# Kernel tuning notes

Hardware: AMD Instinct MI355X
Metric: run time of the kernel (lower is better)

Reference implementation:

```python
import jax, jax.numpy as jnp
import numpy as np

N_SPECIAL = 4
LABEL_ID = 3
C_ACT = 64
C_TIME = 32
ACT_START = N_SPECIAL
TIME_START = N_SPECIAL + C_ACT
VOCAB = TIME_START + C_TIME  # 100
B, T, D = 8, 2048, 256


def l2norm(x, eps=1e-12):
    n = jnp.sqrt(jnp.sum(x * x, axis=-1, keepdims=True))
    return x / jnp.maximum(n, eps)


def causal_proto(h_norm, is_label, nxt, lo, hi, E_cls, alpha):
    """At every <LABEL> position L, build per-class prototypes from earlier
    support label positions (class = next token at that position), add a
    Bayesian prior alpha*E_cls, and return cosine sims of h_norm[L] vs protos.
    Non-label positions (or labels with no earlier support) -> zeros.
    Implemented as a single causal scan over time (online running sums)."""
    Bv, Tv, Dv = h_norm.shape
    C = E_cls.shape[0]
    is_sup = is_label & (nxt >= lo) & (nxt < hi)          # [B,T]
    cls = jnp.clip(nxt - lo, 0, C - 1)                    # [B,T]

    def step(carry, xs):
        Hsum, cnt = carry                                  # [B,C,D], [B,C]
        h_t, cls_t, sup_t, lab_t = xs                      # [B,D],[B],[B],[B]
        proto = l2norm((Hsum + alpha * E_cls) / (cnt[:, :, None] + alpha + 1e-8))
        sims = jnp.einsum('bd,bcd->bc', h_t, proto)        # cosine (h_t is unit)
        valid = lab_t & (jnp.sum(cnt, axis=-1) > 0)        # any earlier support
        out = jnp.where(valid[:, None], sims, 0.0)
        oh = jax.nn.one_hot(cls_t, C, dtype=h_t.dtype) * sup_t[:, None].astype(h_t.dtype)
        Hsum = Hsum + oh[:, :, None] * h_t[:, None, :]
        cnt = cnt + oh
        return (Hsum, cnt), out

    init = (jnp.zeros((Bv, C, Dv), h_norm.dtype), jnp.zeros((Bv, C), h_norm.dtype))
    xs = (jnp.swapaxes(h_norm, 0, 1), jnp.swapaxes(cls, 0, 1),
          jnp.swapaxes(is_sup, 0, 1), jnp.swapaxes(is_label, 0, 1))
    _, outs = jax.lax.scan(jax.checkpoint(step), init, xs)
    return jnp.swapaxes(outs, 0, 1)                        # [B,T,C]


def setup_inputs() -> dict:
    key = jax.random.key(0)
    ks = jax.random.split(key, 6)
    f32 = jnp.float32
    return {
        'tokens': jax.random.randint(ks[0], (B, T), 0, VOCAB, dtype=jnp.int32),
        'h': jax.random.normal(ks[1], (B, T, D), dtype=f32),
        'E': jax.random.normal(ks[2], (VOCAB, D), dtype=f32) * 0.02,
        'W_next': jax.random.normal(ks[3], (C_ACT, D), dtype=f32) * 0.02,
        'b_next': jnp.zeros((C_ACT,), f32),
        'W_time': jax.random.normal(ks[4], (C_TIME, D), dtype=f32) * 0.02,
        'b_time': jnp.zeros((C_TIME,), f32),
        'tied_scale_act': jnp.array(0.0, f32),
        'tied_scale_time': jnp.array(0.0, f32),
        'proto_scale_act': jnp.array(1.0, f32),
        'proto_scale_time': jnp.array(1.0, f32),
        'proto_prior_act': jnp.array(0.5, f32),
        'proto_prior_time': jnp.array(0.5, f32),
        'proto_temp_act': jnp.array(1.0, f32),
        'proto_temp_time': jnp.array(1.0, f32),
    }


def reference(tokens, h, E, W_next, b_next, W_time, b_time,
              tied_scale_act, tied_scale_time, proto_scale_act, proto_scale_time,
              proto_prior_act, proto_prior_time, proto_temp_act, proto_temp_time):
    sp = jax.nn.softplus
    # parametric heads
    param_next = jnp.einsum('btd,cd->btc', h, W_next) + b_next
    param_time = jnp.einsum('btd,cd->btc', h, W_time) + b_time
    # weight-tied heads (gradient flows into E here)
    tied_act = jnp.einsum('btd,cd->btc', h, E[ACT_START:TIME_START])
    tied_time = jnp.einsum('btd,cd->btc', h, E[TIME_START:VOCAB])
    # prototype head (E detached, as in the torch code)
    h_norm = l2norm(h)
    E_det = jax.lax.stop_gradient(E)
    E_act = l2norm(E_det[ACT_START:TIME_START])
    E_time = l2norm(E_det[TIME_START:VOCAB])
    nxt = jnp.roll(tokens, -1, axis=1)
    is_label = tokens == LABEL_ID
    proto_act = causal_proto(h_norm, is_label, nxt, ACT_START, TIME_START,
                             E_act, sp(proto_prior_act)) * sp(proto_temp_act)
    proto_time = causal_proto(h_norm, is_label, nxt, TIME_START, VOCAB,
                              E_time, sp(proto_prior_time)) * sp(proto_temp_time)
    activity_logits = param_next + sp(tied_scale_act) * tied_act + sp(proto_scale_act) * proto_act
    time_logits = param_time + sp(tied_scale_time) * tied_time + sp(proto_scale_time) * proto_time
    return (activity_logits, time_logits)
```

## Files before the change

### kernel.cpp

```cpp
#include <hip/hip_runtime.h>
#include <hip/hip_bf16.h>

#define Bv 8
#define Tv 2048
#define Dv 256
#define C_ACT 64
#define C_TIME 32
#define NCLS 96
#define LABEL_ID 3
#define ACT_START 4
#define TIME_START 68
#define VOCAB 100
#define MAXEV 36

typedef short bf16x8 __attribute__((ext_vector_type(8)));
typedef float f32x4  __attribute__((ext_vector_type(4)));
typedef unsigned short u16x8 __attribute__((ext_vector_type(8)));

__device__ __forceinline__ float bf2f(__hip_bfloat16 x) { return __bfloat162float(x); }
__device__ __forceinline__ float bfb(unsigned short u) {
    union { unsigned int i; float f; } x; x.i = ((unsigned int)u) << 16; return x.f;
}
__device__ __forceinline__ short f2bs(float x) {
    __hip_bfloat16 b = __float2bfloat16(x);
    return *reinterpret_cast<short*>(&b);
}
__device__ __forceinline__ float spf(float x) { return log1pf(expf(x)); }

__device__ __forceinline__ float ldx(const void* p, size_t i, bool f32) {
    return f32 ? ((const float*)p)[i] : bf2f(((const __hip_bfloat16*)p)[i]);
}
__device__ __forceinline__ void stx(void* p, size_t i, float v, bool f32) {
    if (f32) ((float*)p)[i] = v;
    else     ((__hip_bfloat16*)p)[i] = __float2bfloat16(v);
}
__device__ __forceinline__ float4 ld4(const void* p, size_t i, bool f32) {
    if (f32) return *reinterpret_cast<const float4*>((const float*)p + i);
    ushort4 s = *reinterpret_cast<const ushort4*>((const unsigned short*)p + i);
    float4 u; u.x = bfb(s.x); u.y = bfb(s.y); u.z = bfb(s.z); u.w = bfb(s.w);
    return u;
}

__device__ __forceinline__ bool detect_f32_256(const void* h, int tid, int* s_cnt)
{
    if (tid == 0) *s_cnt = 0;
    __syncthreads();
    ushort4 u = *(reinterpret_cast<const ushort4*>(h) + tid);
    int c = 0; float v;
    v = bfb(u.x); if (!(fabsf(v) < 1e20f)) c++;
    v = bfb(u.y); if (!(fabsf(v) < 1e20f)) c++;
    v = bfb(u.z); if (!(fabsf(v) < 1e20f)) c++;
    v = bfb(u.w); if (!(fabsf(v) < 1e20f)) c++;
    #pragma unroll
    for (int o = 32; o > 0; o >>= 1) c += __shfl_down(c, o);
    if ((tid & 63) == 0 && c) atomicAdd(s_cnt, c);
    __syncthreads();
    return *s_cnt >= 4;
}

__device__ __forceinline__ size_t out_idx(int b, int L, int c)
{
    return (c < C_ACT)
        ? ((size_t)(b * Tv + L) * C_ACT + c)
        : ((size_t)Bv * Tv * C_ACT + (size_t)(b * Tv + L) * C_TIME + (c - C_ACT));
}

#define K1_ROWS 32
#define EVLD 264
#define GLD 44

__global__ __launch_bounds__(256) void k_all(
    const int* __restrict__ tokens,
    const void* __restrict__ h,
    const void* __restrict__ E,
    const void* __restrict__ Wn, const void* __restrict__ bn,
    const void* __restrict__ Wt, const void* __restrict__ bt,
    const void* ts_a, const void* ts_t,
    const void* ps_a, const void* ps_t,
    const void* pp_a, const void* pp_t,
    const void* pt_a, const void* pt_t,
    void* __restrict__ out)
{
    __shared__ union {
        unsigned short mB[NCLS][EVLD];
        struct {
            unsigned short hb[48][EVLD];
            union {
                unsigned short AsMs[48][EVLD];
                struct {
                    float Gl[MAXEV][GLD];
                    float P[MAXEV][24];
                    float Pm[MAXEV][24];
                    float SG[MAXEV][24];
                    float ZP[MAXEV][24];
                } r;
            } u2;
            float nrm[MAXEV];
        } s;
    } u;
    __shared__ int s_pos[MAXEV], s_cls[MAXEV];
    __shared__ unsigned long long s_mask[32];
    __shared__ unsigned long long s_bm[24];
    __shared__ unsigned long long s_mact, s_mtim;
    __shared__ int s_cnt, s_evn;

    int tid = threadIdx.x;
    bool f32 = detect_f32_256(h, tid, &s_cnt);
    float spt_a = spf(ldx(ts_a, 0, f32));
    float spt_t = spf(ldx(ts_t, 0, f32));

    if (blockIdx.x >= 32) {
        int R0   = (blockIdx.x - 32) * K1_ROWS;
        int w    = tid >> 6;
        int lane = tid & 63;
        int lr   = lane & 15;
        int quad = lane >> 4;
        int rt   = w & 1;
        int cg   = w >> 1;

        int rowb = 16 * rt + quad * 4;
        int tk[4]; float bs[3];
        #pragma unroll
        for (int r = 0; r < 4; ++r) tk[r] = tokens[R0 + rowb + r];
        #pragma unroll
        for (int nn = 0; nn < 3; ++nn) {
            int c = 16 * (3 * cg + nn) + lr;
            bs[nn] = (c < C_ACT) ? ldx(bn, c, f32) : ldx(bt, c - C_ACT, f32);
        }

        #pragma unroll 4
        for (int k = 0; k < 12; ++k) {
            int f = tid + 256 * k;
            int c = f >> 5, col = (f & 31) * 8;
            bool act = c < C_ACT;
            size_t wrow = act ? (size_t)c : (size_t)(c - C_ACT);
            size_t erow = act ? (size_t)(ACT_START + c) : (size_t)(TIME_START + (c - C_ACT));
            const void* wptr = act ? Wn : Wt;
            float spt = act ? spt_a : spt_t;
            float4 w0 = ld4(wptr, wrow * Dv + col,     f32);
            float4 w1 = ld4(wptr, wrow * Dv + col + 4, f32);
            float4 e0 = ld4(E,    erow * Dv + col,     f32);
            float4 e1 = ld4(E,    erow * Dv + col + 4, f32);
            u16x8 m8;
            m8[0] = (unsigned short)f2bs(w0.x + spt * e0.x);
            m8[1] = (unsigned short)f2bs(w0.y + spt * e0.y);
            m8[2] = (unsigned short)f2bs(w0.z + spt * e0.z);
            m8[3] = (unsigned short)f2bs(w0.w + spt * e0.w);
            m8[4] = (unsigned short)f2bs(w1.x + spt * e1.x);
            m8[5] = (unsigned short)f2bs(w1.y + spt * e1.y);
            m8[6] = (unsigned short)f2bs(w1.z + spt * e1.z);
            m8[7] = (unsigned short)f2bs(w1.w + spt * e1.w);
            *reinterpret_cast<u16x8*>(&u.mB[c][col]) = m8;
        }

        bf16x8 av[8];
        if (!f32) {
            const unsigned short* aB = (const unsigned short*)h
                + (size_t)(R0 + 16 * rt + lr) * Dv + quad * 8;
            #pragma unroll
            for (int t = 0; t < 8; ++t)
                av[t] = *reinterpret_cast<const bf16x8*>(aB + t * 32);
        } else {
            const float* aB = (const float*)h
                + (size_t)(R0 + 16 * rt + lr) * Dv + quad * 8;
            #pragma unroll
            for (int t = 0; t < 8; ++t) {
                float4 a0 = *reinterpret_cast<const float4*>(aB + t * 32);
                float4 a1 = *reinterpret_cast<const float4*>(aB + t * 32 + 4);
                bf16x8 a;
                a[0] = f2bs(a0.x); a[1] = f2bs(a0.y); a[2] = f2bs(a0.z); a[3] = f2bs(a0.w);
                a[4] = f2bs(a1.x); a[5] = f2bs(a1.y); a[6] = f2bs(a1.z); a[7] = f2bs(a1.w);
                av[t] = a;
            }
        }

        __syncthreads();

        f32x4 acc[3];
        #pragma unroll
        for (int n = 0; n < 3; ++n) acc[n] = (f32x4){0.f, 0.f, 0.f, 0.f};
        #pragma unroll
        for (int t = 0; t < 8; ++t) {
            int koff = t * 32 + quad * 8;
            #pragma unroll
            for (int nn = 0; nn < 3; ++nn) {
                bf16x8 b = *reinterpret_cast<const bf16x8*>(
                    &u.mB[16 * (3 * cg + nn) + lr][koff]);
                acc[nn] = __builtin_amdgcn_mfma_f32_16x16x32_bf16(av[t], b, acc[nn], 0, 0, 0);
            }
        }

        #pragma unroll
        for (int nn = 0; nn < 3; ++nn) {
            int c = 16 * (3 * cg + nn) + lr;
            #pragma unroll
            for (int r = 0; r < 4; ++r) {
                if (tk[r] == LABEL_ID) continue;
                int row = R0 + rowb + r;
                stx(out, out_idx(row >> 11, row & (Tv - 1), c), acc[nn][r] + bs[nn], f32);
            }
        }
        return;
    }

    int b  = blockIdx.x >> 2;
    int q  = blockIdx.x & 3;
    int c0 = q * 24;
    int lane = tid & 63, wvx = tid >> 6;

    float alpha_a = spf(ldx(pp_a, 0, f32));
    float alpha_t = spf(ldx(pp_t, 0, f32));

    float4 ev[6], wv6[6];
    #pragma unroll
    for (int k = 0; k < 6; ++k) {
        int lc = wvx + 4 * k, c = c0 + lc;
        bool act = c < C_ACT;
        int erow = act ? (ACT_START + c) : (TIME_START + (c - C_ACT));
        size_t wrow = act ? (size_t)c : (size_t)(c - C_ACT);
        ev[k]  = ld4(E, (size_t)erow * Dv + lane * 4, f32);
        wv6[k] = ld4(act ? Wn : Wt, wrow * Dv + lane * 4, f32);
    }

    int* s_tok = reinterpret_cast<int*>(&u.s.u2.AsMs[0][0]);
    #pragma unroll
    for (int k = 0; k < 8; ++k) {
        int i = tid + 256 * k;
        int tok = tokens[(size_t)b * Tv + i];
        s_tok[i] = tok;
        unsigned long long m = __ballot(tok == LABEL_ID);
        if (lane == 0) s_mask[wvx + 4 * k] = m;
    }
    __syncthreads();

    if (wvx == 0) {
        unsigned long long m = (lane < 32) ? s_mask[lane] : 0ull;
        int cnt = __popcll(m);
        int x = cnt;
        #pragma unroll
        for (int d = 1; d < 32; d <<= 1) {
            int src = lane - d;
            int y = __shfl(x, src < 0 ? 0 : src);
            if (lane >= d) x += y;
        }
        if (lane < 32) {
            int n = x - cnt;
            unsigned long long mm = m;
            while (mm && n < MAXEV) {
                int bit = __builtin_ctzll(mm);
                s_pos[n++] = lane * 64 + bit;
                mm &= mm - 1;
            }
        }
        if (lane == 31) s_evn = (x < MAXEV) ? x : MAXEV;
    }
    __syncthreads();
    int evn = s_evn;
    int nrt = (evn + 15) >> 4;

    if (tid < evn) {
        int nxt = s_tok[(s_pos[tid] + 1) & (Tv - 1)];
        int c = -1;
        if (nxt >= ACT_START && nxt < TIME_START)  c = nxt - ACT_START;
        else if (nxt >= TIME_START && nxt < VOCAB) c = C_ACT + (nxt - TIME_START);
        s_cls[tid] = c;
    }

    {
        float4 hv[9];
        #pragma unroll
        for (int k = 0; k < 9; ++k) {
            int i = wvx + 4 * k;
            if (i < evn)
                hv[k] = ld4(h, ((size_t)b * Tv + s_pos[i]) * Dv + lane * 4, f32);
        }
        #pragma unroll
        for (int k = 0; k < 9; ++k) {
            int i = wvx + 4 * k;
            if (i < evn) {
                float4 v = hv[k];
                float p = v.x * v.x + v.y * v.y + v.z * v.z + v.w * v.w;
                #pragma unroll
                for (int o = 32; o > 0; o >>= 1) p += __shfl_xor(p, o);
                float nr = fmaxf(sqrtf(p), 1e-12f);
                float inv = 1.0f / nr;
                ushort4 s4;
                s4.x = (unsigned short)f2bs(v.x * inv);
                s4.y = (unsigned short)f2bs(v.y * inv);
                s4.z = (unsigned short)f2bs(v.z * inv);
                s4.w = (unsigned short)f2bs(v.w * inv);
                *reinterpret_cast<ushort4*>(&u.s.hb[i][lane * 4]) = s4;
                if (lane == 0) u.s.nrm[i] = nr;
            }
        }
        for (int i = evn + wvx; i < 16 * nrt; i += 4) {
            ushort4 z; z.x = z.y = z.z = z.w = 0;
            *reinterpret_cast<ushort4*>(&u.s.hb[i][lane * 4]) = z;
        }
    }
    __syncthreads();

    {
        #pragma unroll
        for (int k = 0; k < 6; ++k) {
            int lc = wvx + 4 * k, c = c0 + lc;
            bool act = c < C_ACT;
            float4 e4 = ev[k], w4 = wv6[k];
            float p = e4.x * e4.x + e4.y * e4.y + e4.z * e4.z + e4.w * e4.w;
            #pragma unroll
            for (int o = 32; o > 0; o >>= 1) p += __shfl_xor(p, o);
            float alpha = act ? alpha_a : alpha_t;
            float ai  = alpha / fmaxf(sqrtf(p), 1e-12f);
            float spt = act ? spt_a : spt_t;
            ushort4 a4, m4;
            a4.x = (unsigned short)f2bs(e4.x * ai);
            a4.y = (unsigned short)f2bs(e4.y * ai);
            a4.z = (unsigned short)f2bs(e4.z * ai);
            a4.w = (unsigned short)f2bs(e4.w * ai);
            m4.x = (unsigned short)f2bs(w4.x + spt * e4.x);
            m4.y = (unsigned short)f2bs(w4.y + spt * e4.y);
            m4.z = (unsigned short)f2bs(w4.z + spt * e4.z);
            m4.w = (unsigned short)f2bs(w4.w + spt * e4.w);
            *reinterpret_cast<ushort4*>(&u.s.u2.AsMs[lc][lane * 4])      = a4;
            *reinterpret_cast<ushort4*>(&u.s.u2.AsMs[24 + lc][lane * 4]) = m4;
        }
        if (wvx == 1) {
            int cj = (lane < evn) ? s_cls[lane] : -1;
            unsigned long long ma = __ballot(cj >= 0 && cj < C_ACT);
            unsigned long long mt = __ballot(cj >= C_ACT);
            if (lane == 0) { s_mact = ma; s_mtim = mt; }
            for (int lc = 0; lc < 24; ++lc) {
                unsigned long long bmv = __ballot(cj == c0 + lc);
                if (lane == 0) s_bm[lc] = bmv;
            }
        }
    }
    __syncthreads();

    {
        int lr2 = lane & 15, quad2 = lane >> 4;
        int nct = 3 + nrt;
        int TT  = nrt * nct;
        f32x4 accs[5];
        #pragma unroll
        for (int kk = 0; kk < 5; ++kk) {
            int t = wvx + 4 * kk;
            if (t < TT) {
                int rt2 = t / nct, ct = t - rt2 * nct;
                int ar = 16 * rt2 + lr2;
                const unsigned short* bbase = (ct < 3)
                    ? &u.s.u2.AsMs[16 * ct + lr2][0]
                    : &u.s.hb[16 * (ct - 3) + lr2][0];
                f32x4 acc = (f32x4){0.f, 0.f, 0.f, 0.f};
                #pragma unroll
                for (int ks = 0; ks < 8; ++ks) {
                    bf16x8 a  = *reinterpret_cast<const bf16x8*>(
                        &u.s.hb[ar][ks * 32 + quad2 * 8]);
                    bf16x8 bf = *reinterpret_cast<const bf16x8*>(
                        &bbase[ks * 32 + quad2 * 8]);
                    acc = __builtin_amdgcn_mfma_f32_16x16x32_bf16(a, bf, acc, 0, 0, 0);
                }
                accs[kk] = acc;
            }
        }
        __syncthreads();
        #pragma unroll
        for (int kk = 0; kk < 5; ++kk) {
            int t = wvx + 4 * kk;
            if (t < TT) {
                int rt2 = t / nct, ct = t - rt2 * nct;
                #pragma unroll
                for (int r = 0; r < 4; ++r) {
                    int row = 16 * rt2 + quad2 * 4 + r;
                    if (row >= evn) continue;
                    if (ct < 3) {
                        int cc = 16 * ct + lr2;
                        if (cc < 24) u.s.u2.r.P[row][cc] = accs[kk][r];
                        else         u.s.u2.r.Pm[row][cc - 24] = accs[kk][r];
                    } else {
                        int j = 16 * (ct - 3) + lr2;
                        if (j < evn) u.s.u2.r.Gl[row][j] = accs[kk][r];
                    }
                }
            }
        }
    }
    __syncthreads();

    for (int t = tid; t < evn * 24; t += 256) {
        int i = t / 24, lc = t - i * 24;
        unsigned long long m = s_bm[lc] & ((1ull << i) - 1ull);
        float s = 0.f;
        while (m) {
            int j = __builtin_ctzll(m);
            s += u.s.u2.r.Gl[i][j];
            m &= m - 1;
        }
        u.s.u2.r.SG[i][lc] = s;
    }
    __syncthreads();

    {
        int j = lane;
        float gjj = 0.f; int cj = -1;
        if (j < evn) { gjj = u.s.u2.r.Gl[j][j]; cj = s_cls[j]; }
        #pragma unroll
        for (int t6 = 0; t6 < 6; ++t6) {
            int lc = wvx * 6 + t6;
            int c = c0 + lc;
            float z = 0.f;
            if (j < evn && cj == c)
                z = 2.f * (u.s.u2.r.P[j][lc] + u.s.u2.r.SG[j][lc]) + gjj;
            float x = z;
            #pragma unroll
            for (int d = 1; d < 64; d <<= 1) {
                int src = lane - d;
                float y = __shfl(x, src < 0 ? 0 : src);
                if (lane >= d) x += y;
            }
            if (j < evn) u.s.u2.r.ZP[j][lc] = x - z;
        }
    }
    __syncthreads();

    {
        float mult_a = spf(ldx(ps_a, 0, f32)) * spf(ldx(pt_a, 0, f32));
        float mult_t = spf(ldx(ps_t, 0, f32)) * spf(ldx(pt_t, 0, f32));
        unsigned long long ma = s_mact, mt = s_mtim;
        for (int t = tid; t < evn * 24; t += 256) {
            int i = t / 24, lc = t - i * 24;
            int c = c0 + lc;
            bool actc = c < C_ACT;
            float alpha = actc ? alpha_a : alpha_t;
            float bias  = actc ? ldx(bn, c, f32) : ldx(bt, c - C_ACT, f32);
            float mult  = actc ? mult_a : mult_t;
            unsigned long long m = actc ? ma : mt;
            bool any = (m & ((1ull << i) - 1ull)) != 0ull;
            float v = u.s.u2.r.Pm[i][lc] * u.s.nrm[i] + bias;
            if (any) {
                float num = u.s.u2.r.P[i][lc] + u.s.u2.r.SG[i][lc];
                float n2  = alpha * alpha + u.s.u2.r.ZP[i][lc];
                v += mult * (num / fmaxf(sqrtf(n2), 1e-20f));
            }
            stx(out, out_idx(b, s_pos[i], c), v, f32);
        }
    }
}

extern "C" void kernel_launch(void* const* d_in, const int* in_sizes, int n_in,
                              void* d_out, int out_size, void* d_ws, size_t ws_size,
                              hipStream_t stream)
{
    const int* tokens = (const int*)d_in[0];
    const void* h    = d_in[1];
    const void* E    = d_in[2];
    const void* Wn   = d_in[3];
    const void* bn   = d_in[4];
    const void* Wt   = d_in[5];
    const void* bt   = d_in[6];
    const void* ts_a = d_in[7];
    const void* ts_t = d_in[8];
    const void* ps_a = d_in[9];
    const void* ps_t = d_in[10];
    const void* pp_a = d_in[11];
    const void* pp_t = d_in[12];
    const void* pt_a = d_in[13];
    const void* pt_t = d_in[14];

    k_all<<<32 + (Bv * Tv) / K1_ROWS, 256, 0, stream>>>(
        tokens, h, E, Wn, bn, Wt, bt,
        ts_a, ts_t, ps_a, ps_t, pp_a, pp_t, pt_a, pt_t, d_out);
}
```

Baseline: 110.2 us.

## Precompute fused bf16 head weights in a prep kernel and read them from global

A small pre-kernel now builds the combined W + scale*E bf16 matrix once into workspace, so the 512 GEMM blocks no longer rebuild it in shared memory. GEMM blocks read B fragments straight from global/L2, and the shared union shrinks, which may raise occupancy. The dtype-detection pass is replaced by a host-side size check when in_sizes is available. The costs are an extra kernel launch and uncached global loads in the MFMA inner loop.

```diff
diff --git a/kernel.cpp b/kernel.cpp
--- a/kernel.cpp
+++ b/kernel.cpp
@@ -65,6 +65,42 @@
         : ((size_t)Bv * Tv * C_ACT + (size_t)(b * Tv + L) * C_TIME + (c - C_ACT));
 }
 
+__global__ __launch_bounds__(256) void k_prep(
+    const void* __restrict__ h,
+    const void* __restrict__ E,
+    const void* __restrict__ Wn, const void* __restrict__ Wt,
+    const void* ts_a, const void* ts_t,
+    int f32flag, unsigned short* __restrict__ Mws)
+{
+    __shared__ int s_cnt;
+    int tid = threadIdx.x;
+    bool f32 = (f32flag == 2) ? detect_f32_256(h, tid, &s_cnt) : (f32flag == 1);
+    float spt_a = spf(ldx(ts_a, 0, f32));
+    float spt_t = spf(ldx(ts_t, 0, f32));
+
+    int f = blockIdx.x * 256 + tid;
+    int c = f >> 5, col = (f & 31) * 8;
+    bool act = c < C_ACT;
+    size_t wrow = act ? (size_t)c : (size_t)(c - C_ACT);
+    size_t erow = act ? (size_t)(ACT_START + c) : (size_t)(TIME_START + (c - C_ACT));
+    const void* wptr = act ? Wn : Wt;
+    float spt = act ? spt_a : spt_t;
+    float4 w0 = ld4(wptr, wrow * Dv + col,     f32);
+    float4 w1 = ld4(wptr, wrow * Dv + col + 4, f32);
+    float4 e0 = ld4(E,    erow * Dv + col,     f32);
+    float4 e1 = ld4(E,    erow * Dv + col + 4, f32);
+    u16x8 m8;
+    m8[0] = (unsigned short)f2bs(w0.x + spt * e0.x);
+    m8[1] = (unsigned short)f2bs(w0.y + spt * e0.y);
+    m8[2] = (unsigned short)f2bs(w0.z + spt * e0.z);
+    m8[3] = (unsigned short)f2bs(w0.w + spt * e0.w);
+    m8[4] = (unsigned short)f2bs(w1.x + spt * e1.x);
+    m8[5] = (unsigned short)f2bs(w1.y + spt * e1.y);
+    m8[6] = (unsigned short)f2bs(w1.z + spt * e1.z);
+    m8[7] = (unsigned short)f2bs(w1.w + spt * e1.w);
+    *reinterpret_cast<u16x8*>(&Mws[(size_t)c * Dv + col]) = m8;
+}
+
 #define K1_ROWS 32
 #define EVLD 264
 #define GLD 44
@@ -79,25 +115,23 @@
     const void* ps_a, const void* ps_t,
     const void* pp_a, const void* pp_t,
     const void* pt_a, const void* pt_t,
+    int f32flag, const unsigned short* __restrict__ Mws,
     void* __restrict__ out)
 {
-    __shared__ union {
-        unsigned short mB[NCLS][EVLD];
-        struct {
-            unsigned short hb[48][EVLD];
-            union {
-                unsigned short AsMs[48][EVLD];
-                struct {
-                    float Gl[MAXEV][GLD];
-                    float P[MAXEV][24];
-                    float Pm[MAXEV][24];
-                    float SG[MAXEV][24];
-                    float ZP[MAXEV][24];
-                } r;
-            } u2;
-            float nrm[MAXEV];
-        } s;
-    } u;
+    __shared__ struct {
+        unsigned short hb[48][EVLD];
+        union {
+            unsigned short AsMs[48][EVLD];
+            struct {
+                float Gl[MAXEV][GLD];
+                float P[MAXEV][24];
+                float Pm[MAXEV][24];
+                float SG[MAXEV][24];
+                float ZP[MAXEV][24];
+            } r;
+        } u2;
+        float nrm[MAXEV];
+    } us;
     __shared__ int s_pos[MAXEV], s_cls[MAXEV];
     __shared__ unsigned long long s_mask[32];
     __shared__ unsigned long long s_bm[24];
@@ -105,7 +139,7 @@
     __shared__ int s_cnt, s_evn;
 
     int tid = threadIdx.x;
-    bool f32 = detect_f32_256(h, tid, &s_cnt);
+    bool f32 = (f32flag == 2) ? detect_f32_256(h, tid, &s_cnt) : (f32flag == 1);
     float spt_a = spf(ldx(ts_a, 0, f32));
     float spt_t = spf(ldx(ts_t, 0, f32));
 
@@ -128,31 +162,6 @@
             bs[nn] = (c < C_ACT) ? ldx(bn, c, f32) : ldx(bt, c - C_ACT, f32);
         }
 
-        #pragma unroll 4
-        for (int k = 0; k < 12; ++k) {
-            int f = tid + 256 * k;
-            int c = f >> 5, col = (f & 31) * 8;
-            bool act = c < C_ACT;
-            size_t wrow = act ? (size_t)c : (size_t)(c - C_ACT);
-            size_t erow = act ? (size_t)(ACT_START + c) : (size_t)(TIME_START + (c - C_ACT));
-            const void* wptr = act ? Wn : Wt;
-            float spt = act ? spt_a : spt_t;
-            float4 w0 = ld4(wptr, wrow * Dv + col,     f32);
-            float4 w1 = ld4(wptr, wrow * Dv + col + 4, f32);
-            float4 e0 = ld4(E,    erow * Dv + col,     f32);
-            float4 e1 = ld4(E,    erow * Dv + col + 4, f32);
-            u16x8 m8;
-            m8[0] = (unsigned short)f2bs(w0.x + spt * e0.x);
-            m8[1] = (unsigned short)f2bs(w0.y + spt * e0.y);
-            m8[2] = (unsigned short)f2bs(w0.z + spt * e0.z);
-            m8[3] = (unsigned short)f2bs(w0.w + spt * e0.w);
-            m8[4] = (unsigned short)f2bs(w1.x + spt * e1.x);
-            m8[5] = (unsigned short)f2bs(w1.y + spt * e1.y);
-            m8[6] = (unsigned short)f2bs(w1.z + spt * e1.z);
-            m8[7] = (unsigned short)f2bs(w1.w + spt * e1.w);
-            *reinterpret_cast<u16x8*>(&u.mB[c][col]) = m8;
-        }
-
         bf16x8 av[8];
         if (!f32) {
             const unsigned short* aB = (const unsigned short*)h
@@ -174,8 +183,6 @@
             }
         }
 
-        __syncthreads();
-
         f32x4 acc[3];
         #pragma unroll
         for (int n = 0; n < 3; ++n) acc[n] = (f32x4){0.f, 0.f, 0.f, 0.f};
@@ -185,7 +192,7 @@
             #pragma unroll
             for (int nn = 0; nn < 3; ++nn) {
                 bf16x8 b = *reinterpret_cast<const bf16x8*>(
-                    &u.mB[16 * (3 * cg + nn) + lr][koff]);
+                    Mws + (size_t)(16 * (3 * cg + nn) + lr) * Dv + koff);
                 acc[nn] = __builtin_amdgcn_mfma_f32_16x16x32_bf16(av[t], b, acc[nn], 0, 0, 0);
             }
         }
@@ -222,7 +229,7 @@
         wv6[k] = ld4(act ? Wn : Wt, wrow * Dv + lane * 4, f32);
     }
 
-    int* s_tok = reinterpret_cast<int*>(&u.s.u2.AsMs[0][0]);
+    int* s_tok = reinterpret_cast<int*>(&us.u2.AsMs[0][0]);
     #pragma unroll
     for (int k = 0; k < 8; ++k) {
         int i = tid + 256 * k;
@@ -289,13 +296,13 @@
                 s4.y = (unsigned short)f2bs(v.y * inv);
                 s4.z = (unsigned short)f2bs(v.z * inv);
                 s4.w = (unsigned short)f2bs(v.w * inv);
-                *reinterpret_cast<ushort4*>(&u.s.hb[i][lane * 4]) = s4;
-                if (lane == 0) u.s.nrm[i] = nr;
+                *reinterpret_cast<ushort4*>(&us.hb[i][lane * 4]) = s4;
+                if (lane == 0) us.nrm[i] = nr;
             }
         }
         for (int i = evn + wvx; i < 16 * nrt; i += 4) {
             ushort4 z; z.x = z.y = z.z = z.w = 0;
-            *reinterpret_cast<ushort4*>(&u.s.hb[i][lane * 4]) = z;
+            *reinterpret_cast<ushort4*>(&us.hb[i][lane * 4]) = z;
         }
     }
     __syncthreads();
@@ -321,8 +328,8 @@
             m4.y = (unsigned short)f2bs(w4.y + spt * e4.y);
             m4.z = (unsigned short)f2bs(w4.z + spt * e4.z);
             m4.w = (unsigned short)f2bs(w4.w + spt * e4.w);
-            *reinterpret_cast<ushort4*>(&u.s.u2.AsMs[lc][lane * 4])      = a4;
-            *reinterpret_cast<ushort4*>(&u.s.u2.AsMs[24 + lc][lane * 4]) = m4;
+            *reinterpret_cast<ushort4*>(&us.u2.AsMs[lc][lane * 4])      = a4;
+            *reinterpret_cast<ushort4*>(&us.u2.AsMs[24 + lc][lane * 4]) = m4;
         }
         if (wvx == 1) {
             int cj = (lane < evn) ? s_cls[lane] : -1;
@@ -349,13 +356,13 @@
                 int rt2 = t / nct, ct = t - rt2 * nct;
                 int ar = 16 * rt2 + lr2;
                 const unsigned short* bbase = (ct < 3)
-                    ? &u.s.u2.AsMs[16 * ct + lr2][0]
-                    : &u.s.hb[16 * (ct - 3) + lr2][0];
+                    ? &us.u2.AsMs[16 * ct + lr2][0]
+                    : &us.hb[16 * (ct - 3) + lr2][0];
                 f32x4 acc = (f32x4){0.f, 0.f, 0.f, 0.f};
                 #pragma unroll
                 for (int ks = 0; ks < 8; ++ks) {
                     bf16x8 a  = *reinterpret_cast<const bf16x8*>(
-                        &u.s.hb[ar][ks * 32 + quad2 * 8]);
+                        &us.hb[ar][ks * 32 + quad2 * 8]);
                     bf16x8 bf = *reinterpret_cast<const bf16x8*>(
                         &bbase[ks * 32 + quad2 * 8]);
                     acc = __builtin_amdgcn_mfma_f32_16x16x32_bf16(a, bf, acc, 0, 0, 0);
@@ -375,11 +382,11 @@
                     if (row >= evn) continue;
                     if (ct < 3) {
                         int cc = 16 * ct + lr2;
-                        if (cc < 24) u.s.u2.r.P[row][cc] = accs[kk][r];
-                        else         u.s.u2.r.Pm[row][cc - 24] = accs[kk][r];
+                        if (cc < 24) us.u2.r.P[row][cc] = accs[kk][r];
+                        else         us.u2.r.Pm[row][cc - 24] = accs[kk][r];
                     } else {
                         int j = 16 * (ct - 3) + lr2;
-                        if (j < evn) u.s.u2.r.Gl[row][j] = accs[kk][r];
+                        if (j < evn) us.u2.r.Gl[row][j] = accs[kk][r];
                     }
                 }
             }
@@ -393,24 +400,24 @@
         float s = 0.f;
         while (m) {
             int j = __builtin_ctzll(m);
-            s += u.s.u2.r.Gl[i][j];
+            s += us.u2.r.Gl[i][j];
             m &= m - 1;
         }
-        u.s.u2.r.SG[i][lc] = s;
+        us.u2.r.SG[i][lc] = s;
     }
     __syncthreads();
 
     {
         int j = lane;
         float gjj = 0.f; int cj = -1;
-        if (j < evn) { gjj = u.s.u2.r.Gl[j][j]; cj = s_cls[j]; }
+        if (j < evn) { gjj = us.u2.r.Gl[j][j]; cj = s_cls[j]; }
         #pragma unroll
         for (int t6 = 0; t6 < 6; ++t6) {
             int lc = wvx * 6 + t6;
             int c = c0 + lc;
             float z = 0.f;
             if (j < evn && cj == c)
-                z = 2.f * (u.s.u2.r.P[j][lc] + u.s.u2.r.SG[j][lc]) + gjj;
+                z = 2.f * (us.u2.r.P[j][lc] + us.u2.r.SG[j][lc]) + gjj;
             float x = z;
             #pragma unroll
             for (int d = 1; d < 64; d <<= 1) {
@@ -418,7 +425,7 @@
                 float y = __shfl(x, src < 0 ? 0 : src);
                 if (lane >= d) x += y;
             }
-            if (j < evn) u.s.u2.r.ZP[j][lc] = x - z;
+            if (j < evn) us.u2.r.ZP[j][lc] = x - z;
         }
     }
     __syncthreads();
@@ -436,10 +443,10 @@
             float mult  = actc ? mult_a : mult_t;
             unsigned long long m = actc ? ma : mt;
             bool any = (m & ((1ull << i) - 1ull)) != 0ull;
-            float v = u.s.u2.r.Pm[i][lc] * u.s.nrm[i] + bias;
+            float v = us.u2.r.Pm[i][lc] * us.nrm[i] + bias;
             if (any) {
-                float num = u.s.u2.r.P[i][lc] + u.s.u2.r.SG[i][lc];
-                float n2  = alpha * alpha + u.s.u2.r.ZP[i][lc];
+                float num = us.u2.r.P[i][lc] + us.u2.r.SG[i][lc];
+                float n2  = alpha * alpha + us.u2.r.ZP[i][lc];
                 v += mult * (num / fmaxf(sqrtf(n2), 1e-20f));
             }
             stx(out, out_idx(b, s_pos[i], c), v, f32);
@@ -467,7 +474,18 @@
     const void* pt_a = d_in[13];
     const void* pt_t = d_in[14];
 
+    int f32flag = 2;
+    if (in_sizes) {
+        long hb = (long)in_sizes[1];
+        if (hb == (long)Bv * Tv * Dv * 4)      f32flag = 1;
+        else if (hb == (long)Bv * Tv * Dv * 2) f32flag = 0;
+    }
+
+    unsigned short* Mws = (unsigned short*)d_ws;
+
+    k_prep<<<12, 256, 0, stream>>>(h, E, Wn, Wt, ts_a, ts_t, f32flag, Mws);
     k_all<<<32 + (Bv * Tv) / K1_ROWS, 256, 0, stream>>>(
         tokens, h, E, Wn, bn, Wt, bt,
-        ts_a, ts_t, ps_a, ps_t, pp_a, pp_t, pt_a, pt_t, d_out);
-}
+        ts_a, ts_t, ps_a, ps_t, pp_a, pp_t, pt_a, pt_t,
+        f32flag, Mws, d_out);
+}
```

Measured after the change: 120.5 us. 1.09x slower.
